# Performance work log

Measured on AMD Instinct MI355X. Metric: run time of the kernel, lower is better.

The kernel has to match this reference:

```python
import jax, jax.numpy as jnp
import numpy as np

UNITS = 32
BACKBONE = 64

def lecun_tanh(x):
    return 1.7159 * jnp.tanh(0.666 * x)

def setup_inputs() -> dict:
    key = jax.random.key(0)
    ks = jax.random.split(key, 6)
    B, C, T, H, W = 4, 16, 32, 64, 64
    scale_b = 1.0 / np.sqrt(C + UNITS)
    scale_h = 1.0 / np.sqrt(BACKBONE)
    return {
        "x": jax.random.normal(ks[0], (B, C, T, H, W), jnp.float32),
        "Wb": jax.random.normal(ks[1], (BACKBONE, C + UNITS), jnp.float32) * scale_b,
        "bb": jnp.zeros((BACKBONE,), jnp.float32),
        "Wff1": jax.random.normal(ks[2], (UNITS, BACKBONE), jnp.float32) * scale_h,
        "bff1": jnp.zeros((UNITS,), jnp.float32),
        "Wff2": jax.random.normal(ks[3], (UNITS, BACKBONE), jnp.float32) * scale_h,
        "bff2": jnp.zeros((UNITS,), jnp.float32),
        "Wta": jax.random.normal(ks[4], (UNITS, BACKBONE), jnp.float32) * scale_h,
        "bta": jnp.zeros((UNITS,), jnp.float32),
        "Wtb": jax.random.normal(ks[5], (UNITS, BACKBONE), jnp.float32) * scale_h,
        "btb": jnp.zeros((UNITS,), jnp.float32),
    }

def reference(x, Wb, bb, Wff1, bff1, Wff2, bff2, Wta, bta, Wtb, btb):
    # x: (B, C, T, H, W) -> time-major (T, B, C, H, W) for the scan
    xs = jnp.transpose(x, (2, 0, 1, 3, 4))
    B, C, H, W = x.shape[0], x.shape[1], x.shape[3], x.shape[4]
    h0 = jnp.zeros((B, UNITS, H, W), x.dtype)
    ts = jnp.asarray(1.0, x.dtype)  # no timespans provided -> ts = 1.0

    def head(z, Wh, bh):  # channel-wise (1x1) linear: (B,K,H,W) -> (B,U,H,W)
        return jnp.einsum('bkhw,uk->buhw', z, Wh) + bh[None, :, None, None]

    def step(h, xt):
        z = jnp.concatenate([xt, h], axis=1)  # (B, C+U, H, W)
        z = lecun_tanh(jnp.einsum('bchw,kc->bkhw', z, Wb) + bb[None, :, None, None])
        ff1 = jnp.tanh(head(z, Wff1, bff1))
        ff2 = jnp.tanh(head(z, Wff2, bff2))
        t_a = head(z, Wta, bta)
        t_b = head(z, Wtb, btb)
        t_interp = jax.nn.sigmoid(t_a * ts + t_b)
        h_new = ff1 * (1.0 - t_interp) + t_interp * ff2
        return h_new, h_new

    _, ys = jax.lax.scan(step, h0, xs)  # ys: (T, B, U, H, W)
    # stack along dim=1 (batch_first) then permute(0,2,1,3,4) -> (B, U, T, H, W)
    return jnp.transpose(ys, (1, 2, 0, 3, 4))
```

## Files before the change

kernel.cpp:

```cpp
#include <hip/hip_runtime.h>
#include <hip/hip_bf16.h>


#define CIN      16
#define UNITS    32
#define BACKBONE 64
#define CZ       48
#define TSTEPS   32
#define HW       4096
#define NPIX     16
#define NTHREADS 64

typedef __attribute__((ext_vector_type(8))) short  short8;
typedef __attribute__((ext_vector_type(8))) __bf16 bf16x8;
typedef __attribute__((ext_vector_type(4))) float  float4v;
typedef __attribute__((ext_vector_type(4))) unsigned int uint4v;

__device__ __forceinline__ unsigned short bf16_rne(float f) {
    unsigned u = __float_as_uint(f);
    return (unsigned short)((u + 0x7FFFu + ((u >> 16) & 1u)) >> 16);
}
__device__ __forceinline__ float bf16_tof(unsigned short h) {
    return __uint_as_float(((unsigned)h) << 16);
}
__device__ __forceinline__ unsigned cvt_pk_bf16(float lo, float hi) {
    unsigned r;
    asm("v_cvt_pk_bf16_f32 %0, %1, %2" : "=v"(r) : "v"(lo), "v"(hi));
    return r;
}

#if __has_builtin(__builtin_amdgcn_exp2f)
#define EXP2F(x) __builtin_amdgcn_exp2f(x)
#else
#define EXP2F(x) __expf(0.69314718056f * (x))
#endif
#if __has_builtin(__builtin_amdgcn_rcpf)
#define RCPF(x) __builtin_amdgcn_rcpf(x)
#else
#define RCPF(x) __fdividef(1.0f, (x))
#endif

__device__ __forceinline__ float lecun_tanh_f(float v) {
    float e = EXP2F(1.92166925f * v);
    return fmaf(-3.4318f, RCPF(e + 1.0f), 1.7159f);
}
__device__ __forceinline__ float tanh_f(float v) {
    float e = EXP2F(2.88539008f * v);
    return fmaf(-2.0f, RCPF(e + 1.0f), 1.0f);
}
__device__ __forceinline__ float sigmoid_f(float v) {
    float e = EXP2F(-1.44269504f * v);
    return RCPF(1.0f + e);
}
__device__ __forceinline__ float4v mfma16(bf16x8 a, bf16x8 b, float4v c) {
    return __builtin_amdgcn_mfma_f32_16x16x32_bf16(a, b, c, 0, 0, 0);
}
__device__ __forceinline__ void split8(const float* v, bf16x8& hi, bf16x8& lo) {
    short8 sh, sl;
    #pragma unroll
    for (int j = 0; j < 8; ++j) {
        unsigned short h = bf16_rne(v[j]);
        sh[j] = (short)h;
        sl[j] = (short)bf16_rne(v[j] - bf16_tof(h));
    }
    hi = __builtin_bit_cast(bf16x8, sh);
    lo = __builtin_bit_cast(bf16x8, sl);
}

__global__ __launch_bounds__(NTHREADS, 1)
void cfc_mfma_kernel(const float* __restrict__ x,   const float* __restrict__ Wb,
                     const float* __restrict__ bb,
                     const float* __restrict__ Wff1, const float* __restrict__ bff1,
                     const float* __restrict__ Wff2, const float* __restrict__ bff2,
                     const float* __restrict__ Wta,  const float* __restrict__ bta,
                     const float* __restrict__ Wtb,  const float* __restrict__ btb,
                     float* __restrict__ out)
{
    const int lane = threadIdx.x;
    const int ln   = lane & 15;
    const int lq   = lane >> 4;

    const int gpix = blockIdx.x * NPIX;
    const int b    = gpix >> 12;
    const int pinb = gpix & 4095;
    const int px   = pinb + ln;

    bf16x8 Abb_hi[4][2], Abb_lo[4][2];
    #pragma unroll
    for (int mt = 0; mt < 4; ++mt) {
        #pragma unroll
        for (int kt = 0; kt < 2; ++kt) {
            float v[8];
            #pragma unroll
            for (int j = 0; j < 8; ++j) {
                int c = kt * 32 + lq * 8 + j;
                v[j] = (c < CZ) ? Wb[(mt * 16 + ln) * CZ + c] : 0.0f;
            }
            split8(v, Abb_hi[mt][kt], Abb_lo[mt][kt]);
        }
    }
    float bbias[4][4];
    #pragma unroll
    for (int mt = 0; mt < 4; ++mt)
        #pragma unroll
        for (int r = 0; r < 4; ++r)
            bbias[mt][r] = bb[mt * 16 + lq * 4 + r];

    const int head = ln & 3;
    const float* Whp = (head == 0) ? Wff1 : (head == 1) ? Wff2 : (head == 2) ? Wta : Wtb;
    const int urow = (((ln >> 2) + 2) & 3) * 8;
    bf16x8 Ah_hi[8][2], Ah_lo[8][2];
    #pragma unroll
    for (int i = 0; i < 8; ++i) {
        #pragma unroll
        for (int kt = 0; kt < 2; ++kt) {
            float v[8];
            #pragma unroll
            for (int j = 0; j < 8; ++j) {
                int n = 32 * kt + (j >> 2) * 16 + lq * 4 + (j & 3);
                v[j] = Whp[(urow + i) * BACKBONE + n];
            }
            split8(v, Ah_hi[i][kt], Ah_lo[i][kt]);
        }
    }
    const int ub = ((lq + 2) & 3) * 8;
    float hbias[8][4];
    #pragma unroll
    for (int i = 0; i < 8; ++i) {
        int u = ub + i;
        hbias[i][0] = bff1[u]; hbias[i][1] = bff2[u];
        hbias[i][2] = bta[u];  hbias[i][3] = btb[u];
    }

    const int cb = (lq & 1) * 8;
    unsigned xo[8], oo[8];
    #pragma unroll
    for (int j = 0; j < 8; ++j)
        xo[j] = (unsigned)(((b * CIN + cb + j) * TSTEPS) * HW + px);
    #pragma unroll
    for (int i = 0; i < 8; ++i)
        oo[i] = (unsigned)(((b * UNITS + ub + i) * TSTEPS) * HW + px);

    float xa[8], xb2[8];
    #pragma unroll
    for (int j = 0; j < 8; ++j) xa[j] = x[xo[j]];
    unsigned hpk[4] = {0u, 0u, 0u, 0u};
    unsigned toff = 0;

    auto step = [&](int t, float (&xc)[8], float (&xn)[8]) {
        const unsigned tn = toff + ((t < TSTEPS - 1) ? (unsigned)HW : 0u);
        #pragma unroll
        for (int j = 0; j < 8; ++j) xn[j] = x[xo[j] + tn];

        unsigned xpk[4];
        #pragma unroll
        for (int p = 0; p < 4; ++p) xpk[p] = cvt_pk_bf16(xc[2 * p], xc[2 * p + 1]);
        const bool xl = (lq < 2);
        unsigned z0u[4], z1u[4];
        #pragma unroll
        for (int p = 0; p < 4; ++p) {
            z0u[p] = xl ? xpk[p] : hpk[p];
            z1u[p] = xl ? hpk[p] : 0u;
        }
        uint4v zv0 = {z0u[0], z0u[1], z0u[2], z0u[3]};
        uint4v zv1 = {z1u[0], z1u[1], z1u[2], z1u[3]};
        bf16x8 Z0 = __builtin_bit_cast(bf16x8, zv0);
        bf16x8 Z1 = __builtin_bit_cast(bf16x8, zv1);

        float4v acc[4];
        #pragma unroll
        for (int mt = 0; mt < 4; ++mt) {
            float4v a = {bbias[mt][0], bbias[mt][1], bbias[mt][2], bbias[mt][3]};
            a = mfma16(Abb_hi[mt][0], Z0, a);
            a = mfma16(Abb_lo[mt][0], Z0, a);
            a = mfma16(Abb_hi[mt][1], Z1, a);
            a = mfma16(Abb_lo[mt][1], Z1, a);
            acc[mt] = a;
        }

        bf16x8 A2[2];
        #pragma unroll
        for (int kt = 0; kt < 2; ++kt) {
            unsigned w[4];
            #pragma unroll
            for (int h2 = 0; h2 < 2; ++h2) {
                float g0 = lecun_tanh_f(acc[2 * kt + h2][0]);
                float g1 = lecun_tanh_f(acc[2 * kt + h2][1]);
                float g2 = lecun_tanh_f(acc[2 * kt + h2][2]);
                float g3 = lecun_tanh_f(acc[2 * kt + h2][3]);
                w[2 * h2 + 0] = cvt_pk_bf16(g0, g1);
                w[2 * h2 + 1] = cvt_pk_bf16(g2, g3);
            }
            uint4v wv = {w[0], w[1], w[2], w[3]};
            A2[kt] = __builtin_bit_cast(bf16x8, wv);
        }

        float hn[8];
        #pragma unroll
        for (int i = 0; i < 8; ++i) {
            float4v c = {hbias[i][0], hbias[i][1], hbias[i][2], hbias[i][3]};
            c = mfma16(Ah_hi[i][0], A2[0], c);
            c = mfma16(Ah_lo[i][0], A2[0], c);
            c = mfma16(Ah_hi[i][1], A2[1], c);
            c = mfma16(Ah_lo[i][1], A2[1], c);
            float f1 = tanh_f(c[0]);
            float f2 = tanh_f(c[1]);
            float ti = sigmoid_f(c[2] + c[3]);
            float h  = fmaf(ti, f2 - f1, f1);
            out[oo[i] + toff] = h;
            hn[i] = h;
        }
        #pragma unroll
        for (int p = 0; p < 4; ++p) hpk[p] = cvt_pk_bf16(hn[2 * p], hn[2 * p + 1]);
        toff += (unsigned)HW;
    };

    #pragma unroll 1
    for (int t = 0; t < TSTEPS; t += 2) {
        step(t,     xa,  xb2);
        step(t + 1, xb2, xa);
    }
}

extern "C" void kernel_launch(void* const* d_in, const int* in_sizes, int n_in,
                              void* d_out, int out_size, void* d_ws, size_t ws_size,
                              hipStream_t stream) {
    dim3 grid(4 * HW / NPIX);
    cfc_mfma_kernel<<<grid, NTHREADS, 0, stream>>>(
        (const float*)d_in[0], (const float*)d_in[1], (const float*)d_in[2],
        (const float*)d_in[3], (const float*)d_in[4], (const float*)d_in[5],
        (const float*)d_in[6], (const float*)d_in[7], (const float*)d_in[8],
        (const float*)d_in[9], (const float*)d_in[10],
        (float*)d_out);
}
```

Before: 161.3 us.

## Split per-step matmuls across four wavefronts with LDS exchange

New measurement: 171.1 us. +6.1%, slower.

```diff
diff --git a/kernel.cpp b/kernel.cpp
--- a/kernel.cpp
+++ b/kernel.cpp
@@ -9,12 +9,13 @@
 #define TSTEPS   32
 #define HW       4096
 #define NPIX     16
-#define NTHREADS 64
+#define NTHREADS 256
 
 typedef __attribute__((ext_vector_type(8))) short  short8;
 typedef __attribute__((ext_vector_type(8))) __bf16 bf16x8;
 typedef __attribute__((ext_vector_type(4))) float  float4v;
 typedef __attribute__((ext_vector_type(4))) unsigned int uint4v;
+typedef __attribute__((ext_vector_type(2))) unsigned int uint2v;
 
 __device__ __forceinline__ unsigned short bf16_rne(float f) {
     unsigned u = __float_as_uint(f);
@@ -67,7 +68,7 @@
     lo = __builtin_bit_cast(bf16x8, sl);
 }
 
-__global__ __launch_bounds__(NTHREADS, 1)
+__global__ __launch_bounds__(NTHREADS, 4)
 void cfc_mfma_kernel(const float* __restrict__ x,   const float* __restrict__ Wb,
                      const float* __restrict__ bb,
                      const float* __restrict__ Wff1, const float* __restrict__ bff1,
@@ -76,7 +77,12 @@
                      const float* __restrict__ Wtb,  const float* __restrict__ btb,
                      float* __restrict__ out)
 {
-    const int lane = threadIdx.x;
+    __shared__ unsigned abuf[4][64][2];
+    __shared__ unsigned hbuf[4][64];
+
+    const int tid  = threadIdx.x;
+    const int w    = tid >> 6;
+    const int lane = tid & 63;
     const int ln   = lane & 15;
     const int lq   = lane >> 4;
 
@@ -85,72 +91,72 @@
     const int pinb = gpix & 4095;
     const int px   = pinb + ln;
 
-    bf16x8 Abb_hi[4][2], Abb_lo[4][2];
-    #pragma unroll
-    for (int mt = 0; mt < 4; ++mt) {
-        #pragma unroll
-        for (int kt = 0; kt < 2; ++kt) {
-            float v[8];
-            #pragma unroll
-            for (int j = 0; j < 8; ++j) {
-                int c = kt * 32 + lq * 8 + j;
-                v[j] = (c < CZ) ? Wb[(mt * 16 + ln) * CZ + c] : 0.0f;
-            }
-            split8(v, Abb_hi[mt][kt], Abb_lo[mt][kt]);
-        }
-    }
-    float bbias[4][4];
-    #pragma unroll
-    for (int mt = 0; mt < 4; ++mt)
-        #pragma unroll
-        for (int r = 0; r < 4; ++r)
-            bbias[mt][r] = bb[mt * 16 + lq * 4 + r];
+    bf16x8 A1hi[2], A1lo[2];
+    #pragma unroll
+    for (int kt = 0; kt < 2; ++kt) {
+        float v[8];
+        #pragma unroll
+        for (int j = 0; j < 8; ++j) {
+            int c = kt * 32 + lq * 8 + j;
+            v[j] = (c < CZ) ? Wb[(w * 16 + ln) * CZ + c] : 0.0f;
+        }
+        split8(v, A1hi[kt], A1lo[kt]);
+    }
+    float bbias[4];
+    #pragma unroll
+    for (int r = 0; r < 4; ++r) bbias[r] = bb[w * 16 + lq * 4 + r];
 
     const int head = ln & 3;
     const float* Whp = (head == 0) ? Wff1 : (head == 1) ? Wff2 : (head == 2) ? Wta : Wtb;
     const int urow = (((ln >> 2) + 2) & 3) * 8;
-    bf16x8 Ah_hi[8][2], Ah_lo[8][2];
-    #pragma unroll
-    for (int i = 0; i < 8; ++i) {
+    bf16x8 Ah_hi[2][2], Ah_lo[2][2];
+    #pragma unroll
+    for (int i2 = 0; i2 < 2; ++i2) {
+        const int u = urow + 2 * w + i2;
         #pragma unroll
         for (int kt = 0; kt < 2; ++kt) {
             float v[8];
             #pragma unroll
             for (int j = 0; j < 8; ++j) {
                 int n = 32 * kt + (j >> 2) * 16 + lq * 4 + (j & 3);
-                v[j] = Whp[(urow + i) * BACKBONE + n];
+                v[j] = Whp[u * BACKBONE + n];
             }
-            split8(v, Ah_hi[i][kt], Ah_lo[i][kt]);
+            split8(v, Ah_hi[i2][kt], Ah_lo[i2][kt]);
         }
     }
     const int ub = ((lq + 2) & 3) * 8;
-    float hbias[8][4];
-    #pragma unroll
-    for (int i = 0; i < 8; ++i) {
-        int u = ub + i;
-        hbias[i][0] = bff1[u]; hbias[i][1] = bff2[u];
-        hbias[i][2] = bta[u];  hbias[i][3] = btb[u];
+    float hbias[2][4];
+    #pragma unroll
+    for (int i2 = 0; i2 < 2; ++i2) {
+        int u2 = ub + 2 * w + i2;
+        hbias[i2][0] = bff1[u2]; hbias[i2][1] = bff2[u2];
+        hbias[i2][2] = bta[u2];  hbias[i2][3] = btb[u2];
     }
 
     const int cb = (lq & 1) * 8;
-    unsigned xo[8], oo[8];
+    unsigned xo[8], oo[2];
     #pragma unroll
     for (int j = 0; j < 8; ++j)
         xo[j] = (unsigned)(((b * CIN + cb + j) * TSTEPS) * HW + px);
     #pragma unroll
-    for (int i = 0; i < 8; ++i)
-        oo[i] = (unsigned)(((b * UNITS + ub + i) * TSTEPS) * HW + px);
-
+    for (int i2 = 0; i2 < 2; ++i2)
+        oo[i2] = (unsigned)(((b * UNITS + ub + 2 * w + i2) * TSTEPS) * HW + px);
+
+    hbuf[w][lane] = 0u;
     float xa[8], xb2[8];
     #pragma unroll
     for (int j = 0; j < 8; ++j) xa[j] = x[xo[j]];
-    unsigned hpk[4] = {0u, 0u, 0u, 0u};
     unsigned toff = 0;
+    __syncthreads();
 
     auto step = [&](int t, float (&xc)[8], float (&xn)[8]) {
         const unsigned tn = toff + ((t < TSTEPS - 1) ? (unsigned)HW : 0u);
         #pragma unroll
         for (int j = 0; j < 8; ++j) xn[j] = x[xo[j] + tn];
+
+        unsigned hpk[4];
+        #pragma unroll
+        for (int p = 0; p < 4; ++p) hpk[p] = hbuf[p][lane];
 
         unsigned xpk[4];
         #pragma unroll
@@ -167,51 +173,47 @@
         bf16x8 Z0 = __builtin_bit_cast(bf16x8, zv0);
         bf16x8 Z1 = __builtin_bit_cast(bf16x8, zv1);
 
-        float4v acc[4];
-        #pragma unroll
-        for (int mt = 0; mt < 4; ++mt) {
-            float4v a = {bbias[mt][0], bbias[mt][1], bbias[mt][2], bbias[mt][3]};
-            a = mfma16(Abb_hi[mt][0], Z0, a);
-            a = mfma16(Abb_lo[mt][0], Z0, a);
-            a = mfma16(Abb_hi[mt][1], Z1, a);
-            a = mfma16(Abb_lo[mt][1], Z1, a);
-            acc[mt] = a;
-        }
-
-        bf16x8 A2[2];
-        #pragma unroll
-        for (int kt = 0; kt < 2; ++kt) {
-            unsigned w[4];
-            #pragma unroll
-            for (int h2 = 0; h2 < 2; ++h2) {
-                float g0 = lecun_tanh_f(acc[2 * kt + h2][0]);
-                float g1 = lecun_tanh_f(acc[2 * kt + h2][1]);
-                float g2 = lecun_tanh_f(acc[2 * kt + h2][2]);
-                float g3 = lecun_tanh_f(acc[2 * kt + h2][3]);
-                w[2 * h2 + 0] = cvt_pk_bf16(g0, g1);
-                w[2 * h2 + 1] = cvt_pk_bf16(g2, g3);
-            }
-            uint4v wv = {w[0], w[1], w[2], w[3]};
-            A2[kt] = __builtin_bit_cast(bf16x8, wv);
-        }
-
-        float hn[8];
-        #pragma unroll
-        for (int i = 0; i < 8; ++i) {
-            float4v c = {hbias[i][0], hbias[i][1], hbias[i][2], hbias[i][3]};
-            c = mfma16(Ah_hi[i][0], A2[0], c);
-            c = mfma16(Ah_lo[i][0], A2[0], c);
-            c = mfma16(Ah_hi[i][1], A2[1], c);
-            c = mfma16(Ah_lo[i][1], A2[1], c);
+        float4v a = {bbias[0], bbias[1], bbias[2], bbias[3]};
+        a = mfma16(A1hi[0], Z0, a);
+        a = mfma16(A1lo[0], Z0, a);
+        a = mfma16(A1hi[1], Z1, a);
+        a = mfma16(A1lo[1], Z1, a);
+
+        {
+            float g0 = lecun_tanh_f(a[0]);
+            float g1 = lecun_tanh_f(a[1]);
+            float g2 = lecun_tanh_f(a[2]);
+            float g3 = lecun_tanh_f(a[3]);
+            uint2v d = {cvt_pk_bf16(g0, g1), cvt_pk_bf16(g2, g3)};
+            *(uint2v*)&abuf[w][lane][0] = d;
+        }
+        __syncthreads();
+
+        uint2v a01 = *(const uint2v*)&abuf[0][lane][0];
+        uint2v a23 = *(const uint2v*)&abuf[1][lane][0];
+        uint2v a45 = *(const uint2v*)&abuf[2][lane][0];
+        uint2v a67 = *(const uint2v*)&abuf[3][lane][0];
+        uint4v w0 = {a01[0], a01[1], a23[0], a23[1]};
+        uint4v w1 = {a45[0], a45[1], a67[0], a67[1]};
+        bf16x8 A2[2] = {__builtin_bit_cast(bf16x8, w0), __builtin_bit_cast(bf16x8, w1)};
+
+        float hn[2];
+        #pragma unroll
+        for (int i2 = 0; i2 < 2; ++i2) {
+            float4v c = {hbias[i2][0], hbias[i2][1], hbias[i2][2], hbias[i2][3]};
+            c = mfma16(Ah_hi[i2][0], A2[0], c);
+            c = mfma16(Ah_lo[i2][0], A2[0], c);
+            c = mfma16(Ah_hi[i2][1], A2[1], c);
+            c = mfma16(Ah_lo[i2][1], A2[1], c);
             float f1 = tanh_f(c[0]);
             float f2 = tanh_f(c[1]);
             float ti = sigmoid_f(c[2] + c[3]);
             float h  = fmaf(ti, f2 - f1, f1);
-            out[oo[i] + toff] = h;
-            hn[i] = h;
-        }
-        #pragma unroll
-        for (int p = 0; p < 4; ++p) hpk[p] = cvt_pk_bf16(hn[2 * p], hn[2 * p + 1]);
+            out[oo[i2] + toff] = h;
+            hn[i2] = h;
+        }
+        hbuf[w][lane] = cvt_pk_bf16(hn[0], hn[1]);
+        __syncthreads();
         toff += (unsigned)HW;
     };
 
```
